# Optimization experiments

Measured on AMD Instinct MI355X. Metric: run time of the kernel, lower is better.

The kernel has to match this reference:

```python
import jax, jax.numpy as jnp
import numpy as np


def setup_inputs() -> dict:
    key = jax.random.key(0)
    k1, k2, k3 = jax.random.split(key, 3)
    B, T, C = 16, 8192, 256
    inputs = jax.random.normal(k1, (B, T, C), dtype=jnp.float32)
    initial_state = jax.random.normal(k2, (B, C), dtype=jnp.float32)
    # learned smoothing coeff, per-channel, init'd near coeff_init=0.1
    smooth = jax.random.uniform(k3, (C,), dtype=jnp.float32)
    return {"inputs": inputs, "initial_state": initial_state, "smooth": smooth}


def reference(inputs, initial_state, smooth):
    """EMA recurrence y_t = w*x_t + (1-w)*y_{t-1}, vectorized via associative scan.

    inputs: [B, T, C], initial_state: [B, C], smooth: [C].
    The linear recurrence y_t = a*y_{t-1} + b_t (a = 1-w, b_t = w*x_t) is
    computed in O(log T) depth with lax.associative_scan over pairs (a, b),
    composing (a1,b1) then (a2,b2) -> (a1*a2, a2*b1 + b2). The initial state
    is folded in afterwards: y_t = A_t * y_0 + B_t.
    """
    w = jnp.clip(smooth, 0.0, 1.0)                      # [C]
    a = jnp.broadcast_to(1.0 - w, inputs.shape)         # [B, T, C]
    b = w * inputs                                      # [B, T, C]

    def combine(c1, c2):
        a1, b1 = c1
        a2, b2 = c2
        return a1 * a2, a2 * b1 + b2

    A, Bc = jax.lax.associative_scan(combine, (a, b), axis=1)
    return A * initial_state[:, None, :] + Bc           # [B, T, C]
```

## Files before the change

### kernel.cpp

```cpp
#include <hip/hip_runtime.h>


#define CHUNK_L 64

__device__ __forceinline__ float clip01(float v) {
    return fminf(fmaxf(v, 0.0f), 1.0f);
}

__global__ __launch_bounds__(64) void ema_k1_chunk_last(
    const float* __restrict__ x, const float* __restrict__ smooth,
    float* __restrict__ chunk_last, int T, int C, int P) {
    const int blk = blockIdx.x;
    const int b = blk / P;
    const int p = blk - b * P;
    const int c = threadIdx.x << 2;

    float4 w4 = *(const float4*)(smooth + c);
    w4.x = clip01(w4.x); w4.y = clip01(w4.y); w4.z = clip01(w4.z); w4.w = clip01(w4.w);
    const float ax = 1.0f - w4.x, ay = 1.0f - w4.y, az = 1.0f - w4.z, aw = 1.0f - w4.w;

    const int sF4 = C >> 2;
    const float4* xp = (const float4*)(x + ((size_t)b * T + (size_t)p * CHUNK_L) * C) + (c >> 2);

    float y0 = 0.0f, y1 = 0.0f, y2 = 0.0f, y3 = 0.0f;
#pragma unroll 8
    for (int i = 0; i < CHUNK_L; ++i) {
        float4 xv = xp[(size_t)i * sF4];
        y0 = fmaf(ax, y0, w4.x * xv.x);
        y1 = fmaf(ay, y1, w4.y * xv.y);
        y2 = fmaf(az, y2, w4.z * xv.z);
        y3 = fmaf(aw, y3, w4.w * xv.w);
    }
    float4 r; r.x = y0; r.y = y1; r.z = y2; r.w = y3;
    *(float4*)(chunk_last + (size_t)blk * C + c) = r;
}

__global__ void ema_k2_carry_scan(
    const float* __restrict__ chunk_last, const float* __restrict__ init,
    const float* __restrict__ smooth, float* __restrict__ carry_in,
    int C, int P) {
    const int b = blockIdx.x;
    const int c = threadIdx.x;
    const float w = clip01(smooth[c]);
    const float a = 1.0f - w;
    float aL = a;
    for (int e = CHUNK_L; e > 1; e >>= 1) aL *= aL;

    float s = init[(size_t)b * C + c];
    for (int p = 0; p < P; ++p) {
        const size_t idx = ((size_t)b * P + p) * C + c;
        carry_in[idx] = s;
        s = fmaf(aL, s, chunk_last[idx]);
    }
}

__global__ __launch_bounds__(64) void ema_k3_apply(
    const float* __restrict__ x, const float* __restrict__ smooth,
    const float* __restrict__ carry_in, float* __restrict__ out,
    int T, int C, int P) {
    const int blk = blockIdx.x;
    const int b = blk / P;
    const int p = blk - b * P;
    const int c = threadIdx.x << 2;

    float4 w4 = *(const float4*)(smooth + c);
    w4.x = clip01(w4.x); w4.y = clip01(w4.y); w4.z = clip01(w4.z); w4.w = clip01(w4.w);
    const float ax = 1.0f - w4.x, ay = 1.0f - w4.y, az = 1.0f - w4.z, aw = 1.0f - w4.w;

    const float4 s4 = *(const float4*)(carry_in + (size_t)blk * C + c);
    float y0 = s4.x, y1 = s4.y, y2 = s4.z, y3 = s4.w;

    const int sF4 = C >> 2;
    const size_t base = ((size_t)b * T + (size_t)p * CHUNK_L) * C;
    const float4* xp = (const float4*)(x + base) + (c >> 2);
    float4* op = (float4*)(out + base) + (c >> 2);

#pragma unroll 8
    for (int i = 0; i < CHUNK_L; ++i) {
        float4 xv = xp[(size_t)i * sF4];
        y0 = fmaf(ax, y0, w4.x * xv.x);
        y1 = fmaf(ay, y1, w4.y * xv.y);
        y2 = fmaf(az, y2, w4.z * xv.z);
        y3 = fmaf(aw, y3, w4.w * xv.w);
        float4 r; r.x = y0; r.y = y1; r.z = y2; r.w = y3;
        op[(size_t)i * sF4] = r;
    }
}

extern "C" void kernel_launch(void* const* d_in, const int* in_sizes, int n_in,
                              void* d_out, int out_size, void* d_ws, size_t ws_size,
                              hipStream_t stream) {
    const float* x      = (const float*)d_in[0];
    const float* init   = (const float*)d_in[1];
    const float* smooth = (const float*)d_in[2];
    float* out = (float*)d_out;

    const int C  = in_sizes[2];
    const int BC = in_sizes[1];
    const int B  = BC / C;
    const int T  = in_sizes[0] / BC;
    const int P  = T / CHUNK_L;

    float* ws1 = (float*)d_ws;
    float* ws2 = ws1 + (size_t)B * P * C;

    ema_k1_chunk_last<<<dim3(B * P), dim3(C / 4), 0, stream>>>(x, smooth, ws1, T, C, P);
    ema_k2_carry_scan<<<dim3(B), dim3(C), 0, stream>>>(ws1, init, smooth, ws2, C, P);
    ema_k3_apply<<<dim3(B * P), dim3(C / 4), 0, stream>>>(x, smooth, ws2, out, T, C, P);
}
```

Baseline: 290.8 us.

## Fuse carry scan into apply kernel by recomputing per-chunk prefix from chunk tails

Removes the serial per-batch carry-scan kernel. Each apply block now recomputes its incoming state by folding all earlier chunk tails with the decay raised to the chunk length. Loads in both the tail and apply loops are batched eight at a time to expose more memory parallelism. The cost is quadratic redundant reads of the small chunk-tail buffer, which should mostly hit in cache.

```diff
diff --git a/kernel.cpp b/kernel.cpp
--- a/kernel.cpp
+++ b/kernel.cpp
@@ -20,44 +20,29 @@
     const float ax = 1.0f - w4.x, ay = 1.0f - w4.y, az = 1.0f - w4.z, aw = 1.0f - w4.w;
 
     const int sF4 = C >> 2;
-    const float4* xp = (const float4*)(x + ((size_t)b * T + (size_t)p * CHUNK_L) * C) + (c >> 2);
+    const float4* xp = (const float4*)(x + ((size_t)b * T + (size_t)p * CHUNK_L) * C) + threadIdx.x;
 
     float y0 = 0.0f, y1 = 0.0f, y2 = 0.0f, y3 = 0.0f;
-#pragma unroll 8
-    for (int i = 0; i < CHUNK_L; ++i) {
-        float4 xv = xp[(size_t)i * sF4];
-        y0 = fmaf(ax, y0, w4.x * xv.x);
-        y1 = fmaf(ay, y1, w4.y * xv.y);
-        y2 = fmaf(az, y2, w4.z * xv.z);
-        y3 = fmaf(aw, y3, w4.w * xv.w);
+    for (int i0 = 0; i0 < CHUNK_L; i0 += 8) {
+        float4 xv[8];
+#pragma unroll
+        for (int j = 0; j < 8; ++j) xv[j] = xp[(size_t)(i0 + j) * sF4];
+#pragma unroll
+        for (int j = 0; j < 8; ++j) {
+            y0 = fmaf(ax, y0, w4.x * xv[j].x);
+            y1 = fmaf(ay, y1, w4.y * xv[j].y);
+            y2 = fmaf(az, y2, w4.z * xv[j].z);
+            y3 = fmaf(aw, y3, w4.w * xv[j].w);
+        }
     }
     float4 r; r.x = y0; r.y = y1; r.z = y2; r.w = y3;
     *(float4*)(chunk_last + (size_t)blk * C + c) = r;
 }
 
-__global__ void ema_k2_carry_scan(
+__global__ __launch_bounds__(64) void ema_k2_apply(
+    const float* __restrict__ x, const float* __restrict__ smooth,
     const float* __restrict__ chunk_last, const float* __restrict__ init,
-    const float* __restrict__ smooth, float* __restrict__ carry_in,
-    int C, int P) {
-    const int b = blockIdx.x;
-    const int c = threadIdx.x;
-    const float w = clip01(smooth[c]);
-    const float a = 1.0f - w;
-    float aL = a;
-    for (int e = CHUNK_L; e > 1; e >>= 1) aL *= aL;
-
-    float s = init[(size_t)b * C + c];
-    for (int p = 0; p < P; ++p) {
-        const size_t idx = ((size_t)b * P + p) * C + c;
-        carry_in[idx] = s;
-        s = fmaf(aL, s, chunk_last[idx]);
-    }
-}
-
-__global__ __launch_bounds__(64) void ema_k3_apply(
-    const float* __restrict__ x, const float* __restrict__ smooth,
-    const float* __restrict__ carry_in, float* __restrict__ out,
-    int T, int C, int P) {
+    float* __restrict__ out, int T, int C, int P) {
     const int blk = blockIdx.x;
     const int b = blk / P;
     const int p = blk - b * P;
@@ -67,23 +52,51 @@
     w4.x = clip01(w4.x); w4.y = clip01(w4.y); w4.z = clip01(w4.z); w4.w = clip01(w4.w);
     const float ax = 1.0f - w4.x, ay = 1.0f - w4.y, az = 1.0f - w4.z, aw = 1.0f - w4.w;
 
-    const float4 s4 = *(const float4*)(carry_in + (size_t)blk * C + c);
-    float y0 = s4.x, y1 = s4.y, y2 = s4.z, y3 = s4.w;
+    float aLx = ax, aLy = ay, aLz = az, aLw = aw;
+    for (int e = CHUNK_L; e > 1; e >>= 1) { aLx *= aLx; aLy *= aLy; aLz *= aLz; aLw *= aLw; }
+
+    float4 s = *(const float4*)(init + (size_t)b * C + c);
+    const float* cl = chunk_last + (size_t)b * P * C + c;
+    int q = 0;
+    for (; q + 8 <= p; q += 8) {
+        float4 l[8];
+#pragma unroll
+        for (int j = 0; j < 8; ++j) l[j] = *(const float4*)(cl + (size_t)(q + j) * C);
+#pragma unroll
+        for (int j = 0; j < 8; ++j) {
+            s.x = fmaf(aLx, s.x, l[j].x);
+            s.y = fmaf(aLy, s.y, l[j].y);
+            s.z = fmaf(aLz, s.z, l[j].z);
+            s.w = fmaf(aLw, s.w, l[j].w);
+        }
+    }
+    for (; q < p; ++q) {
+        float4 l = *(const float4*)(cl + (size_t)q * C);
+        s.x = fmaf(aLx, s.x, l.x);
+        s.y = fmaf(aLy, s.y, l.y);
+        s.z = fmaf(aLz, s.z, l.z);
+        s.w = fmaf(aLw, s.w, l.w);
+    }
 
     const int sF4 = C >> 2;
     const size_t base = ((size_t)b * T + (size_t)p * CHUNK_L) * C;
-    const float4* xp = (const float4*)(x + base) + (c >> 2);
-    float4* op = (float4*)(out + base) + (c >> 2);
+    const float4* xp = (const float4*)(x + base) + threadIdx.x;
+    float4* op = (float4*)(out + base) + threadIdx.x;
 
-#pragma unroll 8
-    for (int i = 0; i < CHUNK_L; ++i) {
-        float4 xv = xp[(size_t)i * sF4];
-        y0 = fmaf(ax, y0, w4.x * xv.x);
-        y1 = fmaf(ay, y1, w4.y * xv.y);
-        y2 = fmaf(az, y2, w4.z * xv.z);
-        y3 = fmaf(aw, y3, w4.w * xv.w);
-        float4 r; r.x = y0; r.y = y1; r.z = y2; r.w = y3;
-        op[(size_t)i * sF4] = r;
+    float y0 = s.x, y1 = s.y, y2 = s.z, y3 = s.w;
+    for (int i0 = 0; i0 < CHUNK_L; i0 += 8) {
+        float4 xv[8];
+#pragma unroll
+        for (int j = 0; j < 8; ++j) xv[j] = xp[(size_t)(i0 + j) * sF4];
+#pragma unroll
+        for (int j = 0; j < 8; ++j) {
+            y0 = fmaf(ax, y0, w4.x * xv[j].x);
+            y1 = fmaf(ay, y1, w4.y * xv[j].y);
+            y2 = fmaf(az, y2, w4.z * xv[j].z);
+            y3 = fmaf(aw, y3, w4.w * xv[j].w);
+            float4 r; r.x = y0; r.y = y1; r.z = y2; r.w = y3;
+            op[(size_t)(i0 + j) * sF4] = r;
+        }
     }
 }
 
@@ -101,10 +114,8 @@
     const int T  = in_sizes[0] / BC;
     const int P  = T / CHUNK_L;
 
-    float* ws1 = (float*)d_ws;
-    float* ws2 = ws1 + (size_t)B * P * C;
+    float* chunk_last = (float*)d_ws;
 
-    ema_k1_chunk_last<<<dim3(B * P), dim3(C / 4), 0, stream>>>(x, smooth, ws1, T, C, P);
-    ema_k2_carry_scan<<<dim3(B), dim3(C), 0, stream>>>(ws1, init, smooth, ws2, C, P);
-    ema_k3_apply<<<dim3(B * P), dim3(C / 4), 0, stream>>>(x, smooth, ws2, out, T, C, P);
+    ema_k1_chunk_last<<<dim3(B * P), dim3(C / 4), 0, stream>>>(x, smooth, chunk_last, T, C, P);
+    ema_k2_apply<<<dim3(B * P), dim3(C / 4), 0, stream>>>(x, smooth, chunk_last, init, out, T, C, P);
 }
```

Result: faster. 271.2 us (-6.7%).
